# Kernel tuning notes

Hardware: AMD Instinct MI355X
Metric: run time of the kernel (lower is better)

Reference implementation:

```python
import jax, jax.numpy as jnp
import numpy as np

MIN_NORM = 1e-15
EPS = 1e-7
N_NODES = 100000
N_EDGES = 1600000
D_IN = 256
D_OUT = 128

# ---- Hyperboloid manifold ops (HGCN-style) ----

def proj_tan0(u, c):
    # zero out the time (first) coordinate
    return jnp.concatenate([jnp.zeros_like(u[..., :1]), u[..., 1:]], axis=-1)

def proj(x, c):
    # project onto hyperboloid: recompute time coord from space coords
    K = 1.0 / c
    y = x[..., 1:]
    t = jnp.sqrt(jnp.clip(K + jnp.sum(y * y, axis=-1, keepdims=True), EPS, None))
    return jnp.concatenate([t, y], axis=-1)

def expmap0(u, c):
    sqrtK = jnp.sqrt(1.0 / c)
    x = u[..., 1:]
    nrm = jnp.clip(jnp.linalg.norm(x, axis=-1, keepdims=True), MIN_NORM, None)
    theta = nrm / sqrtK
    t0 = sqrtK * jnp.cosh(theta)
    rest = sqrtK * jnp.sinh(theta) * x / nrm
    return proj(jnp.concatenate([t0, rest], axis=-1), c)

def logmap0(x, c):
    sqrtK = jnp.sqrt(1.0 / c)
    y = x[..., 1:]
    nrm = jnp.clip(jnp.linalg.norm(y, axis=-1, keepdims=True), MIN_NORM, None)
    theta = jnp.clip(x[..., :1] / sqrtK, 1.0 + EPS, None)
    rest = sqrtK * jnp.arccosh(theta) * y / nrm
    return jnp.concatenate([jnp.zeros_like(rest[..., :1]), rest], axis=-1)

def mobius_matvec1(m, x, c):
    # weight is (in, out): map via tangent space at origin
    return expmap0(logmap0(x, c) @ m, c)

def mobius_matvec0(n, x, c):
    # per-node scalar (N,1) scaling in tangent space
    return expmap0(n * logmap0(x, c), c)

def mobius_add(x, y, c):
    # tangent-space addition at origin (broadcasts over bias rows)
    return expmap0(logmap0(x, c) + logmap0(y, c), c)

mobius_add0 = mobius_add

def spmm(rows, cols, vals, x):
    # COO sparse adj @ dense x  ->  [N, d]
    return jax.ops.segment_sum(vals[:, None] * x[cols], rows, num_segments=N_NODES)

def gcn_layer(x, weight, bias, rows, cols, vals, c):
    out = mobius_matvec1(weight, x, c)
    hyp_bias = proj(expmap0(proj_tan0(bias[None, :], c), c), c)
    out = mobius_add(out, hyp_bias, c)
    out = logmap0(out, c)
    out = spmm(rows, cols, vals, out)
    return proj(expmap0(out, c), c)


def setup_inputs() -> dict:
    key = jax.random.key(0)
    ks = jax.random.split(key, 12)
    A1_tensor = jax.random.normal(ks[0], (N_NODES, D_IN), dtype=jnp.float32)
    adj_rows = jax.random.randint(ks[1], (N_EDGES,), 0, N_NODES)
    adj_cols = jax.random.randint(ks[2], (N_EDGES,), 0, N_NODES)
    adj_vals = jax.random.uniform(ks[3], (N_EDGES,), dtype=jnp.float32) / 16.0
    raw_c = jnp.full((1,), np.log(np.e - 1.0), dtype=jnp.float32)
    bnd_in = 1.0 / np.sqrt(D_IN)
    bnd_h = 1.0 / np.sqrt(D_OUT)
    Lin1 = jax.random.uniform(ks[4], (D_IN, D_OUT), jnp.float32, -bnd_in, bnd_in)
    Lin1_bias = jax.random.uniform(ks[5], (D_OUT,), jnp.float32, -bnd_in, bnd_in)
    n = jax.random.uniform(ks[6], (N_NODES, 1), jnp.float32, 0.0, 1.0)
    gc1_weight = jax.random.uniform(ks[7], (D_IN, D_OUT), jnp.float32, -bnd_in, bnd_in)
    gc1_bias = jax.random.uniform(ks[8], (D_OUT,), jnp.float32, -bnd_in, bnd_in)
    gc2_weight = jax.random.uniform(ks[9], (D_OUT, D_OUT), jnp.float32, -bnd_h, bnd_h)
    gc2_bias = jax.random.uniform(ks[10], (D_OUT,), jnp.float32, -bnd_h, bnd_h)
    return {"A1_tensor": A1_tensor, "adj_rows": adj_rows, "adj_cols": adj_cols,
            "adj_vals": adj_vals, "raw_c": raw_c, "Lin1": Lin1, "Lin1_bias": Lin1_bias,
            "n": n, "gc1_weight": gc1_weight, "gc1_bias": gc1_bias,
            "gc2_weight": gc2_weight, "gc2_bias": gc2_bias}


def reference(A1_tensor, adj_rows, adj_cols, adj_vals, raw_c, Lin1, Lin1_bias, n,
              gc1_weight, gc1_bias, gc2_weight, gc2_bias):
    c = jax.nn.softplus(raw_c) + 1e-5  # learned curvature, shape (1,)
    # dropout is identity at inference
    x_tan = proj_tan0(A1_tensor, c)
    a = proj(expmap0(x_tan, c), c)
    # skip branch: hyperbolic linear
    a1 = mobius_matvec1(Lin1, a, c)
    hyp_bias = proj(expmap0(proj_tan0(Lin1_bias[None, :], c), c), c)
    a1 = mobius_add(a1, hyp_bias, c)
    a2 = mobius_matvec0(n, a1, c)
    # GCN layer 1 + gated residual
    x_1 = gcn_layer(a, gc1_weight, gc1_bias, adj_rows, adj_cols, adj_vals, c)
    x_1 = mobius_matvec0(1.0 - n, x_1, c)
    x_1 = mobius_add0(x_1, a2, c)
    # GCN layer 2
    x_2 = gcn_layer(x_1, gc2_weight, gc2_bias, adj_rows, adj_cols, adj_vals, c)
    x_2 = logmap0(x_2, c)
    x_2 = jnp.concatenate([x_2, a1], axis=-1)  # [N, 2*D_OUT]
    x_2 = expmap0(x_2, c)
    return (x_2, c)
```

## Files before the change

### kernel.cpp

```cpp
#include <hip/hip_runtime.h>
#include <math.h>


#define NN 100000
#define NP 100096
#define MAXDEG 64
#define NB 391
#define CAP 5120
#define EPT 8
#define EPB 2048

typedef __attribute__((ext_vector_type(8))) short bf16x8;
typedef __attribute__((ext_vector_type(4))) float f32x4;

__device__ __forceinline__ float wsum(float v) {
#pragma unroll
  for (int off = 32; off > 0; off >>= 1) v += __shfl_xor(v, off, 64);
  return v;
}

__device__ __forceinline__ float sane(float v) {
  return fminf(fmaxf(v, -3.0e38f), 3.0e38f);
}

__device__ __forceinline__ float b2f(ushort h) {
  union { unsigned u; float f; } z; z.u = (unsigned)h << 16; return z.f;
}
__device__ __forceinline__ ushort f2b(float f) {
  union { float f; unsigned u; } z; z.f = f;
  unsigned u = z.u;
  unsigned r = (u + 0x7fffu + ((u >> 16) & 1u)) >> 16;
  return (ushort)r;
}

__device__ __forceinline__ void gload16(const void* g, void* l) {
  __builtin_amdgcn_global_load_lds((const __attribute__((address_space(1))) void*)g,
                                   (__attribute__((address_space(3))) void*)l, 16, 0, 0);
}

__global__ __launch_bounds__(256) void prep_kernel(const float* __restrict__ Lin1,
                                                   const float* __restrict__ g1w,
                                                   const float* __restrict__ g2w,
                                                   ushort* __restrict__ Btcat,
                                                   ushort* __restrict__ Btg2,
                                                   int* __restrict__ bucketCnt,
                                                   const float* __restrict__ raw_c,
                                                   float* __restrict__ SC,
                                                   ushort* __restrict__ TBh) {
  int i = blockIdx.x * 256 + threadIdx.x;
  if (i < 65536) {
    int k = i >> 8, n = i & 255;
    float v = (n < 128) ? Lin1[k * 128 + n] : g1w[k * 128 + (n - 128)];
    Btcat[n * 256 + k] = f2b(v);
  } else if (i < 81920) {
    int j = i - 65536, k = j >> 7, n = j & 127;
    Btg2[n * 128 + k] = f2b(g2w[j]);
  } else if (i < 81920 + NB) {
    bucketCnt[i - 81920] = 0;
  } else if (i == 81920 + NB) {
    float rc = raw_c[0];
    float c = fmaxf(rc, 0.0f) + log1pf(expf(-fabsf(rc))) + 1e-5f;
    SC[0] = c;
    SC[1] = 1.0f / c;
    SC[2] = sqrtf(1.0f / c);
    SC[3] = sqrtf(c);
  } else if (i >= 90000 && i < 90000 + 6144) {
    ((unsigned*)(TBh + (size_t)NN * 128))[i - 90000] = 0u;
  }
}

__global__ __launch_bounds__(512) void fused_gemm_kernel(const float* __restrict__ A1,
                                                         const ushort* __restrict__ Btcat,
                                                         ushort* __restrict__ Pb,
                                                         ushort* __restrict__ G1h,
                                                         const float* __restrict__ Lb,
                                                         const float* __restrict__ g1b) {
  __shared__ ushort As[128 * 32];
  __shared__ ushort Bs[256 * 32];
  const int tid = threadIdx.x;
  const int w = tid >> 6, l = tid & 63;
  const int wr = w >> 2, wc = w & 3;
  const int lane16 = l & 15, quad = l >> 4;
  const int bm = blockIdx.x * 128;
  const int swz = (lane16 >> 1) & 3;
  const int ar = tid >> 2;
  const int ak = tid & 3;
  const int akq = ak ^ ((ar >> 1) & 3);
  const int grow = bm + ar;
  f32x4 acc[4][4];
#pragma unroll
  for (int mt = 0; mt < 4; ++mt)
#pragma unroll
    for (int nt = 0; nt < 4; ++nt) acc[mt][nt] = (f32x4){0.f, 0.f, 0.f, 0.f};

  for (int k0 = 0; k0 < 256; k0 += 32) {
#pragma unroll
    for (int p = 0; p < 2; ++p) {
      int sseg = p * 512 + tid;
      int row = sseg >> 2;
      int kq = (sseg & 3) ^ ((row >> 1) & 3);
      int wbase = (p * 512 + (tid & ~63)) * 16;
      gload16(Btcat + (size_t)row * 256 + k0 + kq * 8, (char*)Bs + wbase);
    }
    float4 v0 = make_float4(0.f, 0.f, 0.f, 0.f);
    float4 v1 = make_float4(0.f, 0.f, 0.f, 0.f);
    if (grow < NN) {
      const float* p = A1 + (size_t)grow * 256 + k0 + ak * 8;
      v0 = *(const float4*)p;
      v1 = *(const float4*)(p + 4);
    }
    if (k0 == 0 && ak == 0) v0.x = 0.0f;
    ushort t8[8] = {f2b(v0.x), f2b(v0.y), f2b(v0.z), f2b(v0.w),
                    f2b(v1.x), f2b(v1.y), f2b(v1.z), f2b(v1.w)};
    *(uint4*)(As + ar * 32 + akq * 8) = *(uint4*)t8;
    __syncthreads();
    bf16x8 af[4], bfr[4];
#pragma unroll
    for (int mt = 0; mt < 4; ++mt)
      af[mt] = *(const bf16x8*)((const char*)As +
                (size_t)(wr * 64 + mt * 16 + lane16) * 64 + ((quad ^ swz) * 16));
#pragma unroll
    for (int nt = 0; nt < 4; ++nt)
      bfr[nt] = *(const bf16x8*)((const char*)Bs +
                 (size_t)(wc * 64 + nt * 16 + lane16) * 64 + ((quad ^ swz) * 16));
#pragma unroll
    for (int mt = 0; mt < 4; ++mt)
#pragma unroll
      for (int nt = 0; nt < 4; ++nt)
        acc[mt][nt] = __builtin_amdgcn_mfma_f32_16x16x32_bf16(bfr[nt], af[mt], acc[mt][nt], 0, 0, 0);
    __syncthreads();
  }
#pragma unroll
  for (int nt = 0; nt < 4; ++nt) {
    int colb = wc * 64 + nt * 16 + quad * 4;
    bool isP = colb < 128;
    int cl = isP ? colb : colb - 128;
    float4 b4 = *(const float4*)((isP ? Lb : g1b) + cl);
    if (cl == 0) b4.x = 0.0f;
    ushort* Cp = isP ? Pb : G1h;
#pragma unroll
    for (int mt = 0; mt < 4; ++mt) {
      int row = bm + wr * 64 + mt * 16 + lane16;
      ushort4 st;
      st.x = f2b(acc[mt][nt][0] + b4.x);
      st.y = f2b(acc[mt][nt][1] + b4.y);
      st.z = f2b(acc[mt][nt][2] + b4.z);
      st.w = f2b(acc[mt][nt][3] + b4.w);
      *(ushort4*)(Cp + (size_t)row * 128 + cl) = st;
    }
  }
}

__global__ __launch_bounds__(256) void mfma_gemm_kernel(const ushort* __restrict__ A, int lda,
                                                        const ushort* __restrict__ Bt,
                                                        ushort* __restrict__ C,
                                                        const float* __restrict__ bias,
                                                        int K) {
  __shared__ ushort As[128 * 32];
  __shared__ ushort Bs[128 * 32];
  const int tid = threadIdx.x;
  const int w = tid >> 6, l = tid & 63;
  const int wr = w >> 1, wc = w & 1;
  const int lane16 = l & 15, quad = l >> 4;
  const int bm = blockIdx.x * 128;
  const int swz = (lane16 >> 1) & 3;
  f32x4 acc[4][4];
#pragma unroll
  for (int mt = 0; mt < 4; ++mt)
#pragma unroll
    for (int nt = 0; nt < 4; ++nt) acc[mt][nt] = (f32x4){0.f, 0.f, 0.f, 0.f};

  for (int k0 = 0; k0 < K; k0 += 32) {
#pragma unroll
    for (int p = 0; p < 2; ++p) {
      int sseg = p * 256 + tid;
      int row = sseg >> 2;
      int kq = (sseg & 3) ^ ((row >> 1) & 3);
      int wbase = (p * 256 + (tid & ~63)) * 16;
      gload16(A + (size_t)(bm + row) * lda + k0 + kq * 8, (char*)As + wbase);
      gload16(Bt + (size_t)row * K + k0 + kq * 8, (char*)Bs + wbase);
    }
    __syncthreads();
    bf16x8 af[4], bfr[4];
#pragma unroll
    for (int mt = 0; mt < 4; ++mt)
      af[mt] = *(const bf16x8*)((const char*)As +
                (size_t)(wr * 64 + mt * 16 + lane16) * 64 + ((quad ^ swz) * 16));
#pragma unroll
    for (int nt = 0; nt < 4; ++nt)
      bfr[nt] = *(const bf16x8*)((const char*)Bs +
                 (size_t)(wc * 64 + nt * 16 + lane16) * 64 + ((quad ^ swz) * 16));
#pragma unroll
    for (int mt = 0; mt < 4; ++mt)
#pragma unroll
      for (int nt = 0; nt < 4; ++nt)
        acc[mt][nt] = __builtin_amdgcn_mfma_f32_16x16x32_bf16(bfr[nt], af[mt], acc[mt][nt], 0, 0, 0);
    __syncthreads();
  }
#pragma unroll
  for (int nt = 0; nt < 4; ++nt) {
    int colb = wc * 64 + nt * 16 + quad * 4;
    float4 b4 = *(const float4*)(bias + colb);
    if (colb == 0) b4.x = 0.0f;
#pragma unroll
    for (int mt = 0; mt < 4; ++mt) {
      int row = bm + wr * 64 + mt * 16 + lane16;
      ushort4 st;
      st.x = f2b(acc[mt][nt][0] + b4.x);
      st.y = f2b(acc[mt][nt][1] + b4.y);
      st.z = f2b(acc[mt][nt][2] + b4.z);
      st.w = f2b(acc[mt][nt][3] + b4.w);
      *(ushort4*)(C + (size_t)row * 128 + colb) = st;
    }
  }
}

__global__ __launch_bounds__(256) void part1_kernel(const int* __restrict__ rows,
                                                    const int* __restrict__ cols,
                                                    const float* __restrict__ vals,
                                                    int* __restrict__ bucketCnt,
                                                    uint2* __restrict__ store, int E) {
  __shared__ int hist[NB];
  __shared__ int cursor[NB];
  const int tid = threadIdx.x;
  for (int t = tid; t < NB; t += 256) hist[t] = 0;
  __syncthreads();
  const long base = (long)blockIdx.x * EPB;
  int rw[EPT], ck[EPT];
  float vf[EPT];
#pragma unroll
  for (int k = 0; k < EPT; ++k) {
    long i = base + (long)k * 256 + tid;
    rw[k] = -1;
    if (i < E) { rw[k] = rows[i]; ck[k] = cols[i]; vf[k] = vals[i]; }
  }
#pragma unroll
  for (int k = 0; k < EPT; ++k)
    if (rw[k] >= 0) atomicAdd(&hist[rw[k] >> 8], 1);
  __syncthreads();
  for (int t = tid; t < NB; t += 256) {
    int h = hist[t];
    cursor[t] = (h > 0) ? atomicAdd(&bucketCnt[t], h) : 0;
  }
  __syncthreads();
#pragma unroll
  for (int k = 0; k < EPT; ++k) {
    if (rw[k] >= 0) {
      int b = rw[k] >> 8;
      int pos = atomicAdd(&cursor[b], 1);
      unsigned pk = ((unsigned)ck[k] << 15) | ((unsigned)f2b(vf[k]) & 0x7FFFu);
      if (pos < CAP) store[(size_t)b * CAP + pos] = make_uint2(pk, (unsigned)rw[k]);
    }
  }
}

__global__ __launch_bounds__(1024) void part2_kernel(const int* __restrict__ bucketCnt,
                                                     const uint2* __restrict__ store,
                                                     int* __restrict__ deg,
                                                     unsigned* __restrict__ eCV) {
  __shared__ int d2[256];
  const int b = blockIdx.x, tid = threadIdx.x;
  if (tid < 256) d2[tid] = 0;
  __syncthreads();
  int n = bucketCnt[b];
  n = (n > CAP) ? CAP : n;
  const uint2* bs = store + (size_t)b * CAP;
  for (int i = tid; i < n; i += 1024) {
    uint2 rec = bs[i];
    int rl = rec.y & 255;
    int k = atomicAdd(&d2[rl], 1);
    if (k < MAXDEG) eCV[((size_t)rec.y << 6) + k] = rec.x;
  }
  __syncthreads();
  if (tid < 256) {
    int gr = b * 256 + tid;
    if (gr < NN) {
      int dgv = d2[tid];
      dgv = (dgv > MAXDEG) ? MAXDEG : dgv;
      int pe = (dgv + 15) & ~15;
      for (int k = dgv; k < pe; ++k) eCV[((size_t)gr << 6) + k] = 0u;
      deg[gr] = pe;
    }
  }
}

__device__ __forceinline__ void row_gather(int row, int l,
                                           const int* __restrict__ deg,
                                           const unsigned* __restrict__ eCV,
                                           const ushort* __restrict__ Gh,
                                           float& a0, float& a1) {
  unsigned mine = eCV[(size_t)row * MAXDEG + l];
  int dg = __builtin_amdgcn_readfirstlane(deg[row]);
  a0 = 0.0f; a1 = 0.0f;
  const int lo = l << 1;
  for (int j = 0; j < dg; j += 16) {
    unsigned pj[16];
    ushort2 u[16];
#pragma unroll
    for (int q = 0; q < 16; ++q) {
      pj[q] = (unsigned)__builtin_amdgcn_readlane((int)mine, j + q);
      u[q] = *(const ushort2*)(Gh + ((size_t)(pj[q] >> 15) << 7) + lo);
    }
#pragma unroll
    for (int q = 0; q < 16; ++q) {
      union { unsigned u32; float f; } vv; vv.u32 = (pj[q] & 0x7FFFu) << 16;
      a0 = fmaf(vv.f, b2f(u[q].x), a0);
      a1 = fmaf(vv.f, b2f(u[q].y), a1);
    }
  }
}

__global__ __launch_bounds__(256) void spmm1_kernel(const int* __restrict__ deg,
                                                    const unsigned* __restrict__ eCV,
                                                    const ushort* __restrict__ G1h,
                                                    const ushort* __restrict__ Pb,
                                                    const float* __restrict__ nvec,
                                                    const float* __restrict__ SC,
                                                    ushort* __restrict__ TBh,
                                                    ushort* __restrict__ A1Ph) {
  int row = __builtin_amdgcn_readfirstlane(blockIdx.x * 4 + (threadIdx.x >> 6));
  int l = threadIdx.x & 63;
  if (row >= NN) return;
  float sK = SC[2], rsK = SC[3];
  float nval = nvec[row];
  float a0, a1;
  row_gather(row, l, deg, eCV, G1h, a0, a1);
  ushort2 pu = *(const ushort2*)(Pb + (size_t)row * 128 + 2 * l);
  float p0 = b2f(pu.x), p1 = b2f(pu.y);
  float t10 = (l == 0) ? 0.0f : fmaf(1.0f - nval, a0, nval * p0);
  float t11 = fmaf(1.0f - nval, a1, nval * p1);
  ushort2 tb; tb.x = f2b(t10); tb.y = f2b(t11);
  *(ushort2*)(TBh + (size_t)row * 128 + 2 * l) = tb;
  float px = (l == 0) ? 0.0f : p0;
  float py = p1;
  float ss = wsum(px * px + py * py);
  float rinv = fminf(__builtin_amdgcn_rsqf(ss), 1e15f);
  float nrm = ss * rinv;
  float th = nrm * rsK;
  float e = __expf(th);
  float ei = __builtin_amdgcn_rcpf(e);
  float sh = 0.5f * (e - ei), ch = 0.5f * (e + ei);
  float sc = sK * sh * rinv;
  float t = sK * ch;
  ushort2 st;
  st.x = f2b((l == 0) ? t : sc * px);
  st.y = f2b(sc * py);
  *(ushort2*)(A1Ph + (size_t)row * 128 + 2 * l) = st;
}

__global__ __launch_bounds__(256) void spmm2_kernel(const int* __restrict__ deg,
                                                    const unsigned* __restrict__ eCV,
                                                    const ushort* __restrict__ G2h,
                                                    const ushort* __restrict__ A1Ph,
                                                    const float* __restrict__ SC,
                                                    float* __restrict__ out) {
  int row = __builtin_amdgcn_readfirstlane(blockIdx.x * 4 + (threadIdx.x >> 6));
  int l = threadIdx.x & 63;
  if (row >= NN) return;
  float cval = SC[0], K = SC[1], sK = SC[2], rsK = SC[3];
  float a0, a1;
  row_gather(row, l, deg, eCV, G2h, a0, a1);
  float u0 = (l == 0) ? 0.0f : a0;
  float u1 = a1;
  ushort2 ap = *(const ushort2*)(A1Ph + (size_t)row * 128 + 2 * l);
  float u2 = b2f(ap.x), u3 = b2f(ap.y);
  float ss = wsum(u0 * u0 + u1 * u1 + u2 * u2 + u3 * u3);
  float rinv = fminf(__builtin_amdgcn_rsqf(ss), 1e15f);
  float nrm = ss * rinv;
  float th = nrm * rsK;
  float e = __expf(th);
  float ei = __builtin_amdgcn_rcpf(e);
  float sc = sK * (0.5f * (e - ei)) * rinv;
  float o0 = sc * u0, o1 = sc * u1, o2 = sc * u2, o3 = sc * u3;
  if (l == 0) o0 = 0.0f;
  float t2 = sqrtf(fmaxf(K + sc * sc * ss, 1e-7f));
  float* op = out + (size_t)row * 256;
  float2 w0, w1;
  w0.x = sane((l == 0) ? t2 : o0);
  w0.y = sane(o1);
  w1.x = sane(o2);
  w1.y = sane(o3);
  *(float2*)(op + 2 * l) = w0;
  *(float2*)(op + 128 + 2 * l) = w1;
  if (row == 0 && l == 0) out[(size_t)NN * 256] = cval;
}

extern "C" void kernel_launch(void* const* d_in, const int* in_sizes, int n_in,
                              void* d_out, int out_size, void* d_ws, size_t ws_size,
                              hipStream_t stream) {
  const float* A1  = (const float*)d_in[0];
  const int* rows  = (const int*)d_in[1];
  const int* cols  = (const int*)d_in[2];
  const float* vals = (const float*)d_in[3];
  const float* rawc = (const float*)d_in[4];
  const float* Lin1 = (const float*)d_in[5];
  const float* Lb   = (const float*)d_in[6];
  const float* nv   = (const float*)d_in[7];
  const float* g1w  = (const float*)d_in[8];
  const float* g1b  = (const float*)d_in[9];
  const float* g2w  = (const float*)d_in[10];
  const float* g2b  = (const float*)d_in[11];
  float* out = (float*)d_out;
  float* ws = (float*)d_ws;
  const int E = in_sizes[1];

  float*  SC   = ws;
  ushort* Pb   = (ushort*)(ws + 256);
  ushort* G1h  = Pb + (size_t)128 * NP;
  ushort* TBh  = G1h + (size_t)128 * NP;
  ushort* A1Ph = TBh + (size_t)128 * NP;
  ushort* Btcat = A1Ph + (size_t)128 * NP;
  ushort* Btg2 = Btcat + 256 * 256;
  int* deg      = (int*)(Btg2 + 128 * 128);
  unsigned* eCV = (unsigned*)(deg + NP);
  uint2* store   = (uint2*)A1Ph;
  int* bucketCnt = (int*)(store + (size_t)NB * CAP);

  const int rowBlocks = NN / 4;
  const int gemmGrid = NP / 128;
  const int p1Blocks = (E + EPB - 1) / EPB;
  const int prepBlocks = (90000 + 6144 + 255) / 256;

  prep_kernel<<<prepBlocks, 256, 0, stream>>>(Lin1, g1w, g2w, Btcat, Btg2,
                                              bucketCnt, rawc, SC, TBh);
  part1_kernel<<<p1Blocks, 256, 0, stream>>>(rows, cols, vals, bucketCnt, store, E);
  part2_kernel<<<NB, 1024, 0, stream>>>(bucketCnt, store, deg, eCV);

  fused_gemm_kernel<<<gemmGrid, 512, 0, stream>>>(A1, Btcat, Pb, G1h, Lb, g1b);
  spmm1_kernel<<<rowBlocks, 256, 0, stream>>>(deg, eCV, G1h, Pb, nv, SC, TBh, A1Ph);
  mfma_gemm_kernel<<<gemmGrid, 256, 0, stream>>>(TBh, 128, Btg2, G1h, g2b, 128);
  spmm2_kernel<<<rowBlocks, 256, 0, stream>>>(deg, eCV, G1h, A1Ph, SC, out);
}
```

Baseline: 427.8 us.

## Double-buffer LDS tiles in both MFMA GEMM kernels to overlap loads with compute

Both GEMM kernels now keep two LDS buffers for the A and B tiles. The next k-slice is issued into the spare buffer while MFMAs run on the current one, which removes one of the two barriers per iteration and hides global load latency. In the fused kernel, the A1 fp32 load for the next slice is issued before compute and converted to bf16 afterward. The cost is doubled LDS use, which may reduce occupancy, and higher register pressure.

Measured after the change: 436.0 us. No clear change (+1.9%).

```diff
diff --git a/kernel.cpp b/kernel.cpp
--- a/kernel.cpp
+++ b/kernel.cpp
@@ -75,8 +75,8 @@
                                                          ushort* __restrict__ G1h,
                                                          const float* __restrict__ Lb,
                                                          const float* __restrict__ g1b) {
-  __shared__ ushort As[128 * 32];
-  __shared__ ushort Bs[256 * 32];
+  __shared__ ushort As[2][128 * 32];
+  __shared__ ushort Bs[2][256 * 32];
   const int tid = threadIdx.x;
   const int w = tid >> 6, l = tid & 63;
   const int wr = w >> 2, wc = w & 3;
@@ -87,49 +87,70 @@
   const int ak = tid & 3;
   const int akq = ak ^ ((ar >> 1) & 3);
   const int grow = bm + ar;
+  const bool aval = grow < NN;
+  const float* apb = A1 + (size_t)grow * 256 + ak * 8;
   f32x4 acc[4][4];
 #pragma unroll
   for (int mt = 0; mt < 4; ++mt)
 #pragma unroll
     for (int nt = 0; nt < 4; ++nt) acc[mt][nt] = (f32x4){0.f, 0.f, 0.f, 0.f};
 
-  for (int k0 = 0; k0 < 256; k0 += 32) {
-#pragma unroll
-    for (int p = 0; p < 2; ++p) {
-      int sseg = p * 512 + tid;
-      int row = sseg >> 2;
-      int kq = (sseg & 3) ^ ((row >> 1) & 3);
-      int wbase = (p * 512 + (tid & ~63)) * 16;
-      gload16(Btcat + (size_t)row * 256 + k0 + kq * 8, (char*)Bs + wbase);
-    }
+#define FG_STAGE_B(buf, k0)                                                  \
+  _Pragma("unroll")                                                          \
+  for (int p = 0; p < 2; ++p) {                                              \
+    int sseg = p * 512 + tid;                                                \
+    int row = sseg >> 2;                                                     \
+    int kq = (sseg & 3) ^ ((row >> 1) & 3);                                  \
+    int wbase = (p * 512 + (tid & ~63)) * 16;                                \
+    gload16(Btcat + (size_t)row * 256 + (k0) + kq * 8, (char*)Bs[buf] + wbase); \
+  }
+
+#define FG_COMPUTE(buf)                                                      \
+  {                                                                          \
+    bf16x8 af[4], bfr[4];                                                    \
+    _Pragma("unroll")                                                        \
+    for (int mt = 0; mt < 4; ++mt)                                           \
+      af[mt] = *(const bf16x8*)((const char*)As[buf] +                       \
+                (size_t)(wr * 64 + mt * 16 + lane16) * 64 + ((quad ^ swz) * 16)); \
+    _Pragma("unroll")                                                        \
+    for (int nt = 0; nt < 4; ++nt)                                           \
+      bfr[nt] = *(const bf16x8*)((const char*)Bs[buf] +                      \
+                 (size_t)(wc * 64 + nt * 16 + lane16) * 64 + ((quad ^ swz) * 16)); \
+    _Pragma("unroll")                                                        \
+    for (int mt = 0; mt < 4; ++mt)                                           \
+      _Pragma("unroll")                                                      \
+      for (int nt = 0; nt < 4; ++nt)                                         \
+        acc[mt][nt] = __builtin_amdgcn_mfma_f32_16x16x32_bf16(bfr[nt], af[mt], acc[mt][nt], 0, 0, 0); \
+  }
+
+  FG_STAGE_B(0, 0);
+  {
     float4 v0 = make_float4(0.f, 0.f, 0.f, 0.f);
     float4 v1 = make_float4(0.f, 0.f, 0.f, 0.f);
-    if (grow < NN) {
-      const float* p = A1 + (size_t)grow * 256 + k0 + ak * 8;
-      v0 = *(const float4*)p;
-      v1 = *(const float4*)(p + 4);
-    }
-    if (k0 == 0 && ak == 0) v0.x = 0.0f;
+    if (aval) { v0 = *(const float4*)apb; v1 = *(const float4*)(apb + 4); }
+    if (ak == 0) v0.x = 0.0f;
     ushort t8[8] = {f2b(v0.x), f2b(v0.y), f2b(v0.z), f2b(v0.w),
                     f2b(v1.x), f2b(v1.y), f2b(v1.z), f2b(v1.w)};
-    *(uint4*)(As + ar * 32 + akq * 8) = *(uint4*)t8;
+    *(uint4*)(As[0] + ar * 32 + akq * 8) = *(uint4*)t8;
+  }
+  __syncthreads();
+
+  int buf = 0;
+  for (int t = 0; t < 7; ++t) {
+    const int k1 = (t + 1) * 32;
+    FG_STAGE_B(buf ^ 1, k1);
+    float4 n0 = make_float4(0.f, 0.f, 0.f, 0.f);
+    float4 n1 = make_float4(0.f, 0.f, 0.f, 0.f);
+    if (aval) { n0 = *(const float4*)(apb + k1); n1 = *(const float4*)(apb + k1 + 4); }
+    FG_COMPUTE(buf);
+    ushort t8[8] = {f2b(n0.x), f2b(n0.y), f2b(n0.z), f2b(n0.w),
+                    f2b(n1.x), f2b(n1.y), f2b(n1.z), f2b(n1.w)};
+    *(uint4*)(As[buf ^ 1] + ar * 32 + akq * 8) = *(uint4*)t8;
     __syncthreads();
-    bf16x8 af[4], bfr[4];
-#pragma unroll
-    for (int mt = 0; mt < 4; ++mt)
-      af[mt] = *(const bf16x8*)((const char*)As +
-                (size_t)(wr * 64 + mt * 16 + lane16) * 64 + ((quad ^ swz) * 16));
-#pragma unroll
-    for (int nt = 0; nt < 4; ++nt)
-      bfr[nt] = *(const bf16x8*)((const char*)Bs +
-                 (size_t)(wc * 64 + nt * 16 + lane16) * 64 + ((quad ^ swz) * 16));
-#pragma unroll
-    for (int mt = 0; mt < 4; ++mt)
-#pragma unroll
-      for (int nt = 0; nt < 4; ++nt)
-        acc[mt][nt] = __builtin_amdgcn_mfma_f32_16x16x32_bf16(bfr[nt], af[mt], acc[mt][nt], 0, 0, 0);
-    __syncthreads();
-  }
+    buf ^= 1;
+  }
+  FG_COMPUTE(buf);
+
 #pragma unroll
   for (int nt = 0; nt < 4; ++nt) {
     int colb = wc * 64 + nt * 16 + quad * 4;
@@ -149,6 +170,8 @@
       *(ushort4*)(Cp + (size_t)row * 128 + cl) = st;
     }
   }
+#undef FG_STAGE_B
+#undef FG_COMPUTE
 }
 
 __global__ __launch_bounds__(256) void mfma_gemm_kernel(const ushort* __restrict__ A, int lda,
@@ -156,8 +179,8 @@
                                                         ushort* __restrict__ C,
                                                         const float* __restrict__ bias,
                                                         int K) {
-  __shared__ ushort As[128 * 32];
-  __shared__ ushort Bs[128 * 32];
+  __shared__ ushort As[2][128 * 32];
+  __shared__ ushort Bs[2][128 * 32];
   const int tid = threadIdx.x;
   const int w = tid >> 6, l = tid & 63;
   const int wr = w >> 1, wc = w & 1;
@@ -170,33 +193,47 @@
 #pragma unroll
     for (int nt = 0; nt < 4; ++nt) acc[mt][nt] = (f32x4){0.f, 0.f, 0.f, 0.f};
 
-  for (int k0 = 0; k0 < K; k0 += 32) {
-#pragma unroll
-    for (int p = 0; p < 2; ++p) {
-      int sseg = p * 256 + tid;
-      int row = sseg >> 2;
-      int kq = (sseg & 3) ^ ((row >> 1) & 3);
-      int wbase = (p * 256 + (tid & ~63)) * 16;
-      gload16(A + (size_t)(bm + row) * lda + k0 + kq * 8, (char*)As + wbase);
-      gload16(Bt + (size_t)row * K + k0 + kq * 8, (char*)Bs + wbase);
-    }
+#define MG_STAGE(buf, k0)                                                    \
+  _Pragma("unroll")                                                          \
+  for (int p = 0; p < 2; ++p) {                                              \
+    int sseg = p * 256 + tid;                                                \
+    int row = sseg >> 2;                                                     \
+    int kq = (sseg & 3) ^ ((row >> 1) & 3);                                  \
+    int wbase = (p * 256 + (tid & ~63)) * 16;                                \
+    gload16(A + (size_t)(bm + row) * lda + (k0) + kq * 8, (char*)As[buf] + wbase); \
+    gload16(Bt + (size_t)row * K + (k0) + kq * 8, (char*)Bs[buf] + wbase);   \
+  }
+
+#define MG_COMPUTE(buf)                                                      \
+  {                                                                          \
+    bf16x8 af[4], bfr[4];                                                    \
+    _Pragma("unroll")                                                        \
+    for (int mt = 0; mt < 4; ++mt)                                           \
+      af[mt] = *(const bf16x8*)((const char*)As[buf] +                       \
+                (size_t)(wr * 64 + mt * 16 + lane16) * 64 + ((quad ^ swz) * 16)); \
+    _Pragma("unroll")                                                        \
+    for (int nt = 0; nt < 4; ++nt)                                           \
+      bfr[nt] = *(const bf16x8*)((const char*)Bs[buf] +                      \
+                 (size_t)(wc * 64 + nt * 16 + lane16) * 64 + ((quad ^ swz) * 16)); \
+    _Pragma("unroll")                                                        \
+    for (int mt = 0; mt < 4; ++mt)                                           \
+      _Pragma("unroll")                                                      \
+      for (int nt = 0; nt < 4; ++nt)                                         \
+        acc[mt][nt] = __builtin_amdgcn_mfma_f32_16x16x32_bf16(bfr[nt], af[mt], acc[mt][nt], 0, 0, 0); \
+  }
+
+  MG_STAGE(0, 0);
+  __syncthreads();
+  int buf = 0;
+  const int nsteps = K >> 5;
+  for (int t = 0; t < nsteps - 1; ++t) {
+    MG_STAGE(buf ^ 1, (t + 1) * 32);
+    MG_COMPUTE(buf);
     __syncthreads();
-    bf16x8 af[4], bfr[4];
-#pragma unroll
-    for (int mt = 0; mt < 4; ++mt)
-      af[mt] = *(const bf16x8*)((const char*)As +
-                (size_t)(wr * 64 + mt * 16 + lane16) * 64 + ((quad ^ swz) * 16));
-#pragma unroll
-    for (int nt = 0; nt < 4; ++nt)
-      bfr[nt] = *(const bf16x8*)((const char*)Bs +
-                 (size_t)(wc * 64 + nt * 16 + lane16) * 64 + ((quad ^ swz) * 16));
-#pragma unroll
-    for (int mt = 0; mt < 4; ++mt)
-#pragma unroll
-      for (int nt = 0; nt < 4; ++nt)
-        acc[mt][nt] = __builtin_amdgcn_mfma_f32_16x16x32_bf16(bfr[nt], af[mt], acc[mt][nt], 0, 0, 0);
-    __syncthreads();
-  }
+    buf ^= 1;
+  }
+  MG_COMPUTE(buf);
+
 #pragma unroll
   for (int nt = 0; nt < 4; ++nt) {
     int colb = wc * 64 + nt * 16 + quad * 4;
@@ -213,6 +250,8 @@
       *(ushort4*)(C + (size_t)row * 128 + colb) = st;
     }
   }
+#undef MG_STAGE
+#undef MG_COMPUTE
 }
 
 __global__ __launch_bounds__(256) void part1_kernel(const int* __restrict__ rows,
```

## Load GEMM operands directly from global memory into MFMA fragments, dropping LDS staging

Applied to the files above, without the earlier changes.

Both GEMM kernels stop staging A and B tiles through shared memory with barriers. Each lane now loads its MFMA fragment straight from global memory, and the fused kernel converts fp32 activations to bf16 in registers using packed conversion. This removes LDS traffic and __syncthreads stalls. In exchange, operands shared across waves are fetched redundantly through L1/L2 and reads are less coalesced, since each lane reads 16-32 bytes from a different row.

New measurement: 497.0 us. +16.2%, slower.

```diff
diff --git a/kernel.cpp b/kernel.cpp
--- a/kernel.cpp
+++ b/kernel.cpp
@@ -1,4 +1,5 @@
 #include <hip/hip_runtime.h>
+#include <hip/hip_bf16.h>
 #include <math.h>
 
 
@@ -32,10 +33,9 @@
   unsigned r = (u + 0x7fffu + ((u >> 16) & 1u)) >> 16;
   return (ushort)r;
 }
-
-__device__ __forceinline__ void gload16(const void* g, void* l) {
-  __builtin_amdgcn_global_load_lds((const __attribute__((address_space(1))) void*)g,
-                                   (__attribute__((address_space(3))) void*)l, 16, 0, 0);
+__device__ __forceinline__ unsigned f2x2(float a, float b) {
+  __hip_bfloat162 h = __float22bfloat162_rn(make_float2(a, b));
+  union { __hip_bfloat162 h; unsigned u; } z; z.h = h; return z.u;
 }
 
 __global__ __launch_bounds__(256) void prep_kernel(const float* __restrict__ Lin1,
@@ -75,61 +75,54 @@
                                                          ushort* __restrict__ G1h,
                                                          const float* __restrict__ Lb,
                                                          const float* __restrict__ g1b) {
-  __shared__ ushort As[128 * 32];
-  __shared__ ushort Bs[256 * 32];
   const int tid = threadIdx.x;
   const int w = tid >> 6, l = tid & 63;
   const int wr = w >> 2, wc = w & 3;
   const int lane16 = l & 15, quad = l >> 4;
   const int bm = blockIdx.x * 128;
-  const int swz = (lane16 >> 1) & 3;
-  const int ar = tid >> 2;
-  const int ak = tid & 3;
-  const int akq = ak ^ ((ar >> 1) & 3);
-  const int grow = bm + ar;
+  const float* apt[4];
+  const ushort* bpt[4];
+#pragma unroll
+  for (int mt = 0; mt < 4; ++mt) {
+    int r = bm + wr * 64 + mt * 16 + lane16;
+    r = (r < NN) ? r : (NN - 1);
+    apt[mt] = A1 + (size_t)r * 256 + quad * 8;
+  }
+#pragma unroll
+  for (int nt = 0; nt < 4; ++nt) {
+    int cn = wc * 64 + nt * 16 + lane16;
+    bpt[nt] = Btcat + (size_t)cn * 256 + quad * 8;
+  }
   f32x4 acc[4][4];
 #pragma unroll
   for (int mt = 0; mt < 4; ++mt)
 #pragma unroll
     for (int nt = 0; nt < 4; ++nt) acc[mt][nt] = (f32x4){0.f, 0.f, 0.f, 0.f};
 
-  for (int k0 = 0; k0 < 256; k0 += 32) {
-#pragma unroll
-    for (int p = 0; p < 2; ++p) {
-      int sseg = p * 512 + tid;
-      int row = sseg >> 2;
-      int kq = (sseg & 3) ^ ((row >> 1) & 3);
-      int wbase = (p * 512 + (tid & ~63)) * 16;
-      gload16(Btcat + (size_t)row * 256 + k0 + kq * 8, (char*)Bs + wbase);
-    }
-    float4 v0 = make_float4(0.f, 0.f, 0.f, 0.f);
-    float4 v1 = make_float4(0.f, 0.f, 0.f, 0.f);
-    if (grow < NN) {
-      const float* p = A1 + (size_t)grow * 256 + k0 + ak * 8;
-      v0 = *(const float4*)p;
-      v1 = *(const float4*)(p + 4);
-    }
-    if (k0 == 0 && ak == 0) v0.x = 0.0f;
-    ushort t8[8] = {f2b(v0.x), f2b(v0.y), f2b(v0.z), f2b(v0.w),
-                    f2b(v1.x), f2b(v1.y), f2b(v1.z), f2b(v1.w)};
-    *(uint4*)(As + ar * 32 + akq * 8) = *(uint4*)t8;
-    __syncthreads();
+#pragma unroll
+  for (int t = 0; t < 8; ++t) {
+    const int k0 = t * 32;
     bf16x8 af[4], bfr[4];
 #pragma unroll
-    for (int mt = 0; mt < 4; ++mt)
-      af[mt] = *(const bf16x8*)((const char*)As +
-                (size_t)(wr * 64 + mt * 16 + lane16) * 64 + ((quad ^ swz) * 16));
+    for (int mt = 0; mt < 4; ++mt) {
+      float4 v0 = *(const float4*)(apt[mt] + k0);
+      float4 v1 = *(const float4*)(apt[mt] + k0 + 4);
+      unsigned q0 = f2x2(v0.x, v0.y), q1 = f2x2(v0.z, v0.w);
+      unsigned q2 = f2x2(v1.x, v1.y), q3 = f2x2(v1.z, v1.w);
+      if (t == 0 && quad == 0) q0 &= 0xFFFF0000u;
+      uint4 u = make_uint4(q0, q1, q2, q3);
+      af[mt] = *(bf16x8*)&u;
+    }
 #pragma unroll
     for (int nt = 0; nt < 4; ++nt)
-      bfr[nt] = *(const bf16x8*)((const char*)Bs +
-                 (size_t)(wc * 64 + nt * 16 + lane16) * 64 + ((quad ^ swz) * 16));
+      bfr[nt] = *(const bf16x8*)(bpt[nt] + k0);
 #pragma unroll
     for (int mt = 0; mt < 4; ++mt)
 #pragma unroll
       for (int nt = 0; nt < 4; ++nt)
         acc[mt][nt] = __builtin_amdgcn_mfma_f32_16x16x32_bf16(bfr[nt], af[mt], acc[mt][nt], 0, 0, 0);
-    __syncthreads();
-  }
+  }
+
 #pragma unroll
   for (int nt = 0; nt < 4; ++nt) {
     int colb = wc * 64 + nt * 16 + quad * 4;
@@ -156,47 +149,39 @@
                                                         ushort* __restrict__ C,
                                                         const float* __restrict__ bias,
                                                         int K) {
-  __shared__ ushort As[128 * 32];
-  __shared__ ushort Bs[128 * 32];
   const int tid = threadIdx.x;
   const int w = tid >> 6, l = tid & 63;
   const int wr = w >> 1, wc = w & 1;
   const int lane16 = l & 15, quad = l >> 4;
   const int bm = blockIdx.x * 128;
-  const int swz = (lane16 >> 1) & 3;
+  const ushort* apt[4];
+  const ushort* bpt[4];
+#pragma unroll
+  for (int mt = 0; mt < 4; ++mt)
+    apt[mt] = A + (size_t)(bm + wr * 64 + mt * 16 + lane16) * lda + quad * 8;
+#pragma unroll
+  for (int nt = 0; nt < 4; ++nt)
+    bpt[nt] = Bt + (size_t)(wc * 64 + nt * 16 + lane16) * K + quad * 8;
   f32x4 acc[4][4];
 #pragma unroll
   for (int mt = 0; mt < 4; ++mt)
 #pragma unroll
     for (int nt = 0; nt < 4; ++nt) acc[mt][nt] = (f32x4){0.f, 0.f, 0.f, 0.f};
 
+#pragma unroll 4
   for (int k0 = 0; k0 < K; k0 += 32) {
-#pragma unroll
-    for (int p = 0; p < 2; ++p) {
-      int sseg = p * 256 + tid;
-      int row = sseg >> 2;
-      int kq = (sseg & 3) ^ ((row >> 1) & 3);
-      int wbase = (p * 256 + (tid & ~63)) * 16;
-      gload16(A + (size_t)(bm + row) * lda + k0 + kq * 8, (char*)As + wbase);
-      gload16(Bt + (size_t)row * K + k0 + kq * 8, (char*)Bs + wbase);
-    }
-    __syncthreads();
     bf16x8 af[4], bfr[4];
 #pragma unroll
-    for (int mt = 0; mt < 4; ++mt)
-      af[mt] = *(const bf16x8*)((const char*)As +
-                (size_t)(wr * 64 + mt * 16 + lane16) * 64 + ((quad ^ swz) * 16));
-#pragma unroll
-    for (int nt = 0; nt < 4; ++nt)
-      bfr[nt] = *(const bf16x8*)((const char*)Bs +
-                 (size_t)(wc * 64 + nt * 16 + lane16) * 64 + ((quad ^ swz) * 16));
+    for (int mt = 0; mt < 4; ++mt) af[mt] = *(const bf16x8*)(apt[mt] + k0);
+#pragma unroll
+    for (int nt = 0; nt < 4; ++nt) bfr[nt] = *(const bf16x8*)(bpt[nt] + k0);
 #pragma unroll
     for (int mt = 0; mt < 4; ++mt)
 #pragma unroll
       for (int nt = 0; nt < 4; ++nt)
         acc[mt][nt] = __builtin_amdgcn_mfma_f32_16x16x32_bf16(bfr[nt], af[mt], acc[mt][nt], 0, 0, 0);
-    __syncthreads();
-  }
+  }
+
 #pragma unroll
   for (int nt = 0; nt < 4; ++nt) {
     int colb = wc * 64 + nt * 16 + quad * 4;
```
